# Performance work log

Measured on AMD Instinct MI355X. Metric: run time of the kernel, lower is better.

Reference implementation:

```python
import jax, jax.numpy as jnp
import numpy as np

B, T, F, H, E = 32, 512, 64, 64, 32  # batch, time, features(=sequence_length), hidden_dim, encoding_size


def setup_inputs() -> dict:
    key = jax.random.key(0)
    ks = jax.random.split(key, 14)
    sc = 0.05
    return {
        "x": jax.random.normal(ks[0], (B, T, F), jnp.float32),
        "s": jax.random.normal(ks[1], (B, T, E), jnp.float32),
        # gating FFN params
        "ffn_w1": jax.random.normal(ks[2], (F, H), jnp.float32) * sc,
        "ffn_b1": jnp.zeros((H,), jnp.float32),
        "ffn_w2": jax.random.normal(ks[3], (E, H), jnp.float32) * sc,
        "ffn_b2": jnp.zeros((H,), jnp.float32),
        "ffn_w3": jax.random.normal(ks[4], (H, F), jnp.float32) * sc,
        "ffn_b3": jnp.zeros((F,), jnp.float32),
        # per-feature expert FFN_j params (F experts, each Dense(1->H), ELU, Dense(H->H))
        "exp_w1": jax.random.normal(ks[5], (F, H), jnp.float32) * sc,  # weight of Dense(1->H) per feature
        "exp_b1": jnp.zeros((F, H), jnp.float32),
        "exp_w3": jax.random.normal(ks[6], (F, H, H), jnp.float32) * sc,
        "exp_b3": jnp.zeros((F, H), jnp.float32),
    }


def reference(x, s, ffn_w1, ffn_b1, ffn_w2, ffn_b2, ffn_w3, ffn_b3,
              exp_w1, exp_b1, exp_w3, exp_b3):
    # gating network: softmax over feature axis
    g = jnp.einsum('btf,fh->bth', x, ffn_w1) + ffn_b1 \
        + jnp.einsum('bte,eh->bth', s, ffn_w2) + ffn_b2
    logits = jnp.einsum('bth,hf->btf', jax.nn.elu(g), ffn_w3) + ffn_b3
    w_t = jax.nn.softmax(logits, axis=2)  # [B,T,F]

    # per-feature experts, batched: Dense(1->H) is a rank-1 outer product
    h = jax.nn.elu(x[..., None] * exp_w1[None, None] + exp_b1[None, None])  # [B,T,F,H]
    expert_out = jnp.einsum('btfh,fhk->btfk', h, exp_w3) + exp_b3[None, None]  # [B,T,F,H]

    # gate-weighted sum over features
    return jnp.einsum('btfk,btf->btk', expert_out, w_t)  # [B,T,H]
```

## Files before the change

kernel.cpp:

```cpp
#include <hip/hip_runtime.h>
#include <hip/hip_bf16.h>
#include <math.h>

#define NTOK 16384

typedef __attribute__((ext_vector_type(8))) short short8;
typedef __attribute__((ext_vector_type(4))) float f32x4;

__device__ __forceinline__ unsigned pack_bf16(float a, float b) {
    union { __hip_bfloat162 h; unsigned u; } cv;
    cv.h = __float22bfloat162_rn(make_float2(a, b));
    return cv.u;
}
__device__ __forceinline__ float eluf(float z) {
    return z > 0.0f ? z : (__expf(z) - 1.0f);
}

__global__ __launch_bounds__(256)
void prepass(const float* __restrict__ ew3, const float* __restrict__ eb3,
             unsigned short* __restrict__ ws) {
    __shared__ float tile[64 * 65];
    const int bid = blockIdx.x, tid = threadIdx.x;
    const float* src = (bid < 64) ? (ew3 + (size_t)bid * 4096) : eb3;

    const int r = tid >> 2, c0 = (tid & 3) * 16;
    #pragma unroll
    for (int j = 0; j < 4; ++j) {
        float4 v = *(const float4*)(src + r * 64 + c0 + j * 4);
        tile[r * 65 + c0 + j * 4 + 0] = v.x;
        tile[r * 65 + c0 + j * 4 + 1] = v.y;
        tile[r * 65 + c0 + j * 4 + 2] = v.z;
        tile[r * 65 + c0 + j * 4 + 3] = v.w;
    }
    __syncthreads();

    uint4* dst = (uint4*)(ws + (size_t)bid * 4096);
    #pragma unroll
    for (int it = 0; it < 2; ++it) {
        const int idx = tid + it * 256;
        const int c = idx >> 8, u = (idx >> 6) & 3, l = idx & 63;
        const int m = l & 15, q = (l >> 4) & 3;
        const int rb = c * 32 + q * 8, col = u * 16 + m;
        unsigned pw[4];
        #pragma unroll
        for (int p = 0; p < 4; ++p)
            pw[p] = pack_bf16(tile[(rb + 2 * p) * 65 + col],
                              tile[(rb + 2 * p + 1) * 65 + col]);
        uint4 pk; pk.x = pw[0]; pk.y = pw[1]; pk.z = pw[2]; pk.w = pw[3];
        dst[idx] = pk;
    }
}

__device__ __forceinline__ void gen_a(const float* __restrict__ ew1,
                                      const float* __restrict__ eb1,
                                      int f, int quad, float xv, float wt,
                                      short8* a) {
    #pragma unroll
    for (int c = 0; c < 2; ++c) {
        const float* w1p = ew1 + f * 64 + c * 32 + quad * 8;
        const float* b1p = eb1 + f * 64 + c * 32 + quad * 8;
        const float4 w1a = *(const float4*)w1p, w1b = *(const float4*)(w1p + 4);
        const float4 b1a = *(const float4*)b1p, b1b = *(const float4*)(b1p + 4);
        uint4 av;
        av.x = pack_bf16(wt * eluf(fmaf(xv, w1a.x, b1a.x)),
                         wt * eluf(fmaf(xv, w1a.y, b1a.y)));
        av.y = pack_bf16(wt * eluf(fmaf(xv, w1a.z, b1a.z)),
                         wt * eluf(fmaf(xv, w1a.w, b1a.w)));
        av.z = pack_bf16(wt * eluf(fmaf(xv, w1b.x, b1b.x)),
                         wt * eluf(fmaf(xv, w1b.y, b1b.y)));
        av.w = pack_bf16(wt * eluf(fmaf(xv, w1b.z, b1b.z)),
                         wt * eluf(fmaf(xv, w1b.w, b1b.w)));
        a[c] = *(short8*)&av;
    }
}

__device__ __forceinline__ void gen_b_fp32(const float* __restrict__ w3f,
                                           int quad, int m, short8 b[2][4]) {
    #pragma unroll
    for (int c = 0; c < 2; ++c)
        #pragma unroll
        for (int u = 0; u < 4; ++u) {
            const float* wp = w3f + (size_t)(c * 32 + quad * 8) * 64 + u * 16 + m;
            uint4 v;
            v.x = pack_bf16(wp[0],   wp[64]);
            v.y = pack_bf16(wp[128], wp[192]);
            v.z = pack_bf16(wp[256], wp[320]);
            v.w = pack_bf16(wp[384], wp[448]);
            b[c][u] = *(short8*)&v;
        }
}

__global__ __launch_bounds__(512, 8)
void moe_main(const float* __restrict__ x,   const float* __restrict__ s,
              const float* __restrict__ fw1, const float* __restrict__ fb1,
              const float* __restrict__ fw2, const float* __restrict__ fb2,
              const float* __restrict__ fw3, const float* __restrict__ fb3,
              const float* __restrict__ ew1, const float* __restrict__ eb1,
              const float* __restrict__ ew3, const float* __restrict__ eb3,
              const unsigned short* __restrict__ w3img, int use_ws,
              float* __restrict__ out)
{
    __shared__ __align__(16) float xls[16 * 68];
    __shared__ __align__(16) float wts[16 * 65];
    __shared__ __align__(16) float egs[16 * 64];
    __shared__ __align__(16) float ped[4][16 * 68];

    const int tid = threadIdx.x;
    const int wv = tid >> 6, lane = tid & 63;
    const int tokbase = blockIdx.x * 16;

    if (tid < 256) {
        const int t = tid >> 4, fq = (tid & 15) * 4;
        *(float4*)&xls[t * 68 + fq] =
            *(const float4*)(x + (size_t)(tokbase + t) * 64 + fq);
    }
    __syncthreads();

    {
        const int t0w = wv * 2;
        const float* sw = s + (size_t)(tokbase + t0w) * 32;
        float g0, g1;
        g0 = g1 = fb1[lane] + fb2[lane];
        for (int f = 0; f < 64; f += 4) {
            const float4 xa = *(const float4*)&xls[(t0w + 0) * 68 + f];
            const float4 xb = *(const float4*)&xls[(t0w + 1) * 68 + f];
            const float w0 = fw1[(f + 0) * 64 + lane];
            const float w1 = fw1[(f + 1) * 64 + lane];
            const float w2 = fw1[(f + 2) * 64 + lane];
            const float w3v = fw1[(f + 3) * 64 + lane];
            g0 = fmaf(xa.x, w0, fmaf(xa.y, w1, fmaf(xa.z, w2, fmaf(xa.w, w3v, g0))));
            g1 = fmaf(xb.x, w0, fmaf(xb.y, w1, fmaf(xb.z, w2, fmaf(xb.w, w3v, g1))));
        }
        for (int e = 0; e < 32; e += 4) {
            const float4 sa = *(const float4*)(sw + e);
            const float4 sb = *(const float4*)(sw + 32 + e);
            const float w0 = fw2[(e + 0) * 64 + lane];
            const float w1 = fw2[(e + 1) * 64 + lane];
            const float w2 = fw2[(e + 2) * 64 + lane];
            const float w3v = fw2[(e + 3) * 64 + lane];
            g0 = fmaf(sa.x, w0, fmaf(sa.y, w1, fmaf(sa.z, w2, fmaf(sa.w, w3v, g0))));
            g1 = fmaf(sb.x, w0, fmaf(sb.y, w1, fmaf(sb.z, w2, fmaf(sb.w, w3v, g1))));
        }
        egs[(t0w + 0) * 64 + lane] = eluf(g0);
        egs[(t0w + 1) * 64 + lane] = eluf(g1);
        __syncthreads();

        float lg0 = fb3[lane], lg1 = lg0;
        for (int h = 0; h < 64; h += 4) {
            const float4 e0 = *(const float4*)&egs[(t0w + 0) * 64 + h];
            const float4 e1 = *(const float4*)&egs[(t0w + 1) * 64 + h];
            const float w0 = fw3[(h + 0) * 64 + lane];
            const float w1 = fw3[(h + 1) * 64 + lane];
            const float w2 = fw3[(h + 2) * 64 + lane];
            const float w3v = fw3[(h + 3) * 64 + lane];
            lg0 = fmaf(e0.x, w0, fmaf(e0.y, w1, fmaf(e0.z, w2, fmaf(e0.w, w3v, lg0))));
            lg1 = fmaf(e1.x, w0, fmaf(e1.y, w1, fmaf(e1.z, w2, fmaf(e1.w, w3v, lg1))));
        }
        float mx0 = lg0, mx1 = lg1;
        #pragma unroll
        for (int off = 32; off > 0; off >>= 1) {
            mx0 = fmaxf(mx0, __shfl_xor(mx0, off));
            mx1 = fmaxf(mx1, __shfl_xor(mx1, off));
        }
        const float p0 = __expf(lg0 - mx0), p1 = __expf(lg1 - mx1);
        float s0 = p0, s1 = p1;
        #pragma unroll
        for (int off = 32; off > 0; off >>= 1) {
            s0 += __shfl_xor(s0, off);
            s1 += __shfl_xor(s1, off);
        }
        wts[(t0w + 0) * 65 + lane] = p0 / s0;
        wts[(t0w + 1) * 65 + lane] = p1 / s1;
    }
    __syncthreads();

    const int m = tid & 15, quad = (tid >> 4) & 3;
    const int f0 = wv * 8;

    f32x4 acc[4];
    #pragma unroll
    for (int u = 0; u < 4; ++u) acc[u] = (f32x4){0.f, 0.f, 0.f, 0.f};

    if (use_ws) {
        const uint4* bb = (const uint4*)w3img;
        #pragma unroll
        for (int ff = 0; ff < 8; ++ff) {
            const int f = f0 + ff;
            const uint4* bp = bb + (size_t)f * 512;
            const float xv = xls[m * 68 + f];
            const float wt = wts[m * 65 + f];
            short8 a[2];
            gen_a(ew1, eb1, f, quad, xv, wt, a);
            {
                uint4 b0 = bp[0 * 256 + 0 * 64 + lane];
                uint4 b1 = bp[0 * 256 + 1 * 64 + lane];
                uint4 b2 = bp[0 * 256 + 2 * 64 + lane];
                uint4 b3 = bp[0 * 256 + 3 * 64 + lane];
                acc[0] = __builtin_amdgcn_mfma_f32_16x16x32_bf16(a[0], *(short8*)&b0, acc[0], 0, 0, 0);
                acc[1] = __builtin_amdgcn_mfma_f32_16x16x32_bf16(a[0], *(short8*)&b1, acc[1], 0, 0, 0);
                acc[2] = __builtin_amdgcn_mfma_f32_16x16x32_bf16(a[0], *(short8*)&b2, acc[2], 0, 0, 0);
                acc[3] = __builtin_amdgcn_mfma_f32_16x16x32_bf16(a[0], *(short8*)&b3, acc[3], 0, 0, 0);
            }
            {
                uint4 b0 = bp[1 * 256 + 0 * 64 + lane];
                uint4 b1 = bp[1 * 256 + 1 * 64 + lane];
                uint4 b2 = bp[1 * 256 + 2 * 64 + lane];
                uint4 b3 = bp[1 * 256 + 3 * 64 + lane];
                acc[0] = __builtin_amdgcn_mfma_f32_16x16x32_bf16(a[1], *(short8*)&b0, acc[0], 0, 0, 0);
                acc[1] = __builtin_amdgcn_mfma_f32_16x16x32_bf16(a[1], *(short8*)&b1, acc[1], 0, 0, 0);
                acc[2] = __builtin_amdgcn_mfma_f32_16x16x32_bf16(a[1], *(short8*)&b2, acc[2], 0, 0, 0);
                acc[3] = __builtin_amdgcn_mfma_f32_16x16x32_bf16(a[1], *(short8*)&b3, acc[3], 0, 0, 0);
            }
        }
    } else {
        for (int ff = 0; ff < 8; ++ff) {
            const int f = f0 + ff;
            short8 b[2][4], a[2];
            gen_b_fp32(ew3 + (size_t)f * 4096, quad, m, b);
            gen_a(ew1, eb1, f, quad, xls[m * 68 + f], wts[m * 65 + f], a);
            #pragma unroll
            for (int u = 0; u < 4; ++u) {
                acc[u] = __builtin_amdgcn_mfma_f32_16x16x32_bf16(a[0], b[0][u], acc[u], 0, 0, 0);
                acc[u] = __builtin_amdgcn_mfma_f32_16x16x32_bf16(a[1], b[1][u], acc[u], 0, 0, 0);
            }
        }
    }

    if (wv < 2) {
        const int e0 = wv * 32 + quad * 8;
        uint4 av;
        av.x = pack_bf16(wts[m * 65 + e0 + 0], wts[m * 65 + e0 + 1]);
        av.y = pack_bf16(wts[m * 65 + e0 + 2], wts[m * 65 + e0 + 3]);
        av.z = pack_bf16(wts[m * 65 + e0 + 4], wts[m * 65 + e0 + 5]);
        av.w = pack_bf16(wts[m * 65 + e0 + 6], wts[m * 65 + e0 + 7]);
        short8 a = *(short8*)&av;
        short8 b[4];
        if (use_ws) {
            const uint4* bp = (const uint4*)(w3img + (size_t)64 * 4096);
            #pragma unroll
            for (int u = 0; u < 4; ++u) {
                uint4 bv = bp[wv * 256 + u * 64 + lane];
                b[u] = *(short8*)&bv;
            }
        } else {
            #pragma unroll
            for (int u = 0; u < 4; ++u) {
                const float* wp = eb3 + (size_t)e0 * 64 + u * 16 + m;
                uint4 bv;
                bv.x = pack_bf16(wp[0],   wp[64]);
                bv.y = pack_bf16(wp[128], wp[192]);
                bv.z = pack_bf16(wp[256], wp[320]);
                bv.w = pack_bf16(wp[384], wp[448]);
                b[u] = *(short8*)&bv;
            }
        }
        #pragma unroll
        for (int u = 0; u < 4; ++u)
            acc[u] = __builtin_amdgcn_mfma_f32_16x16x32_bf16(a, b[u], acc[u], 0, 0, 0);
    }

    if (wv >= 4) {
        #pragma unroll
        for (int u = 0; u < 4; ++u)
            #pragma unroll
            for (int r = 0; r < 4; ++r)
                ped[wv - 4][(quad * 4 + r) * 68 + u * 16 + m] = acc[u][r];
    }
    __syncthreads();
    if (wv < 4) {
        #pragma unroll
        for (int u = 0; u < 4; ++u)
            #pragma unroll
            for (int r = 0; r < 4; ++r)
                acc[u][r] += ped[wv][(quad * 4 + r) * 68 + u * 16 + m];
    }
    __syncthreads();
    if (wv == 2 || wv == 3) {
        #pragma unroll
        for (int u = 0; u < 4; ++u)
            #pragma unroll
            for (int r = 0; r < 4; ++r)
                ped[wv - 2][(quad * 4 + r) * 68 + u * 16 + m] = acc[u][r];
    }
    __syncthreads();
    if (wv < 2) {
        #pragma unroll
        for (int u = 0; u < 4; ++u)
            #pragma unroll
            for (int r = 0; r < 4; ++r)
                acc[u][r] += ped[wv][(quad * 4 + r) * 68 + u * 16 + m];
    }
    __syncthreads();
    if (wv == 1) {
        #pragma unroll
        for (int u = 0; u < 4; ++u)
            #pragma unroll
            for (int r = 0; r < 4; ++r)
                ped[0][(quad * 4 + r) * 68 + u * 16 + m] = acc[u][r];
    }
    __syncthreads();
    if (wv == 0) {
        #pragma unroll
        for (int u = 0; u < 4; ++u)
            #pragma unroll
            for (int r = 0; r < 4; ++r) {
                const int idx = (quad * 4 + r) * 68 + u * 16 + m;
                ped[0][idx] += acc[u][r];
            }
    }
    __syncthreads();

    if (tid < 256) {
        const int t = tid >> 4, kq = tid & 15;
        float4 o = *(const float4*)&ped[0][t * 68 + kq * 4];
        *(float4*)(out + (size_t)(tokbase + t) * 64 + kq * 4) = o;
    }
}

extern "C" void kernel_launch(void* const* d_in, const int* in_sizes, int n_in,
                              void* d_out, int out_size, void* d_ws, size_t ws_size,
                              hipStream_t stream) {
    const float* x   = (const float*)d_in[0];
    const float* s   = (const float*)d_in[1];
    const float* fw1 = (const float*)d_in[2];
    const float* fb1 = (const float*)d_in[3];
    const float* fw2 = (const float*)d_in[4];
    const float* fb2 = (const float*)d_in[5];
    const float* fw3 = (const float*)d_in[6];
    const float* fb3 = (const float*)d_in[7];
    const float* ew1 = (const float*)d_in[8];
    const float* eb1 = (const float*)d_in[9];
    const float* ew3 = (const float*)d_in[10];
    const float* eb3 = (const float*)d_in[11];
    float* out = (float*)d_out;

    const size_t ws_need = (size_t)65 * 4096 * sizeof(unsigned short);
    const int use_ws = (ws_size >= ws_need) && (((uintptr_t)d_ws & 15) == 0);
    unsigned short* w3img = (unsigned short*)d_ws;

    if (use_ws) prepass<<<dim3(65), dim3(256), 0, stream>>>(ew3, eb3, w3img);
    moe_main<<<dim3(NTOK / 16), dim3(512), 0, stream>>>(
        x, s, fw1, fb1, fw2, fb2, fw3, fb3, ew1, eb1, ew3, eb3,
        w3img, use_ws, out);
}
```

Baseline: 130.2 us.

## Split MoE into gate prep, feature-parallel expert kernel with register-resident weights, and reduction

Result: slower. 447.2 us (+243.5%).

```diff
diff --git a/kernel.cpp b/kernel.cpp
--- a/kernel.cpp
+++ b/kernel.cpp
@@ -3,6 +3,10 @@
 #include <math.h>
 
 #define NTOK 16384
+#define WTS_OFF   532480
+#define P_OFF     4726784
+#define NSLOT_F32 1048576
+#define WS_NEED   (size_t)(P_OFF + 9 * 4194304)
 
 typedef __attribute__((ext_vector_type(8))) short short8;
 typedef __attribute__((ext_vector_type(4))) float f32x4;
@@ -17,44 +21,275 @@
 }
 
 __global__ __launch_bounds__(256)
-void prepass(const float* __restrict__ ew3, const float* __restrict__ eb3,
-             unsigned short* __restrict__ ws) {
-    __shared__ float tile[64 * 65];
-    const int bid = blockIdx.x, tid = threadIdx.x;
-    const float* src = (bid < 64) ? (ew3 + (size_t)bid * 4096) : eb3;
-
-    const int r = tid >> 2, c0 = (tid & 3) * 16;
-    #pragma unroll
-    for (int j = 0; j < 4; ++j) {
-        float4 v = *(const float4*)(src + r * 64 + c0 + j * 4);
-        tile[r * 65 + c0 + j * 4 + 0] = v.x;
-        tile[r * 65 + c0 + j * 4 + 1] = v.y;
-        tile[r * 65 + c0 + j * 4 + 2] = v.z;
-        tile[r * 65 + c0 + j * 4 + 3] = v.w;
-    }
-    __syncthreads();
-
-    uint4* dst = (uint4*)(ws + (size_t)bid * 4096);
-    #pragma unroll
-    for (int it = 0; it < 2; ++it) {
-        const int idx = tid + it * 256;
-        const int c = idx >> 8, u = (idx >> 6) & 3, l = idx & 63;
-        const int m = l & 15, q = (l >> 4) & 3;
-        const int rb = c * 32 + q * 8, col = u * 16 + m;
-        unsigned pw[4];
-        #pragma unroll
-        for (int p = 0; p < 4; ++p)
-            pw[p] = pack_bf16(tile[(rb + 2 * p) * 65 + col],
-                              tile[(rb + 2 * p + 1) * 65 + col]);
-        uint4 pk; pk.x = pw[0]; pk.y = pw[1]; pk.z = pw[2]; pk.w = pw[3];
-        dst[idx] = pk;
-    }
-}
-
-__device__ __forceinline__ void gen_a(const float* __restrict__ ew1,
-                                      const float* __restrict__ eb1,
-                                      int f, int quad, float xv, float wt,
-                                      short8* a) {
+void gate_prep(const float* __restrict__ x,   const float* __restrict__ s,
+               const float* __restrict__ fw1, const float* __restrict__ fb1,
+               const float* __restrict__ fw2, const float* __restrict__ fb2,
+               const float* __restrict__ fw3, const float* __restrict__ fb3,
+               const float* __restrict__ ew3, const float* __restrict__ eb3,
+               unsigned short* __restrict__ img,
+               float* __restrict__ wtsb, float* __restrict__ p8)
+{
+    __shared__ __align__(16) float xls[16 * 68];
+    __shared__ __align__(16) float wts[16 * 65];
+    __shared__ __align__(16) float egs[16 * 64];
+    __shared__ __align__(16) float ptile[64 * 65];
+
+    const int tid = threadIdx.x, bid = blockIdx.x;
+
+    if (bid < 65) {
+        const float* src = (bid < 64) ? (ew3 + (size_t)bid * 4096) : eb3;
+        const int r = tid >> 2, c0 = (tid & 3) * 16;
+        #pragma unroll
+        for (int j = 0; j < 4; ++j) {
+            float4 v = *(const float4*)(src + r * 64 + c0 + j * 4);
+            ptile[r * 65 + c0 + j * 4 + 0] = v.x;
+            ptile[r * 65 + c0 + j * 4 + 1] = v.y;
+            ptile[r * 65 + c0 + j * 4 + 2] = v.z;
+            ptile[r * 65 + c0 + j * 4 + 3] = v.w;
+        }
+        __syncthreads();
+        uint4* dst = (uint4*)(img + (size_t)bid * 4096);
+        #pragma unroll
+        for (int it = 0; it < 2; ++it) {
+            const int idx = it * 256 + tid;
+            const int c = idx >> 8, u = (idx >> 6) & 3, l = idx & 63;
+            const int mm = l & 15, q = (l >> 4) & 3;
+            const int rb = c * 32 + q * 8, col = u * 16 + mm;
+            unsigned pw[4];
+            #pragma unroll
+            for (int p = 0; p < 4; ++p)
+                pw[p] = pack_bf16(ptile[(rb + 2 * p) * 65 + col],
+                                  ptile[(rb + 2 * p + 1) * 65 + col]);
+            uint4 pk; pk.x = pw[0]; pk.y = pw[1]; pk.z = pw[2]; pk.w = pw[3];
+            dst[idx] = pk;
+        }
+        return;
+    }
+
+    const int wv = tid >> 6, lane = tid & 63;
+    const int tokbase = (bid - 65) * 16;
+
+    if (tid < 256) {
+        const int t = tid >> 4, fq = (tid & 15) * 4;
+        *(float4*)&xls[t * 68 + fq] =
+            *(const float4*)(x + (size_t)(tokbase + t) * 64 + fq);
+    }
+    __syncthreads();
+
+    {
+        const int t0w = wv * 4;
+        const float* sw = s + (size_t)(tokbase + t0w) * 32;
+        float g[4];
+        const float b0 = fb1[lane] + fb2[lane];
+        #pragma unroll
+        for (int t = 0; t < 4; ++t) g[t] = b0;
+        for (int f = 0; f < 64; f += 4) {
+            const float w0 = fw1[(f + 0) * 64 + lane];
+            const float w1 = fw1[(f + 1) * 64 + lane];
+            const float w2 = fw1[(f + 2) * 64 + lane];
+            const float w3v = fw1[(f + 3) * 64 + lane];
+            #pragma unroll
+            for (int t = 0; t < 4; ++t) {
+                const float4 xa = *(const float4*)&xls[(t0w + t) * 68 + f];
+                g[t] = fmaf(xa.x, w0, fmaf(xa.y, w1, fmaf(xa.z, w2, fmaf(xa.w, w3v, g[t]))));
+            }
+        }
+        for (int e = 0; e < 32; e += 4) {
+            const float w0 = fw2[(e + 0) * 64 + lane];
+            const float w1 = fw2[(e + 1) * 64 + lane];
+            const float w2 = fw2[(e + 2) * 64 + lane];
+            const float w3v = fw2[(e + 3) * 64 + lane];
+            #pragma unroll
+            for (int t = 0; t < 4; ++t) {
+                const float4 sa = *(const float4*)(sw + t * 32 + e);
+                g[t] = fmaf(sa.x, w0, fmaf(sa.y, w1, fmaf(sa.z, w2, fmaf(sa.w, w3v, g[t]))));
+            }
+        }
+        #pragma unroll
+        for (int t = 0; t < 4; ++t) egs[(t0w + t) * 64 + lane] = eluf(g[t]);
+
+        float lg[4];
+        const float b3 = fb3[lane];
+        #pragma unroll
+        for (int t = 0; t < 4; ++t) lg[t] = b3;
+        for (int h = 0; h < 64; h += 4) {
+            const float w0 = fw3[(h + 0) * 64 + lane];
+            const float w1 = fw3[(h + 1) * 64 + lane];
+            const float w2 = fw3[(h + 2) * 64 + lane];
+            const float w3v = fw3[(h + 3) * 64 + lane];
+            #pragma unroll
+            for (int t = 0; t < 4; ++t) {
+                const float4 ev = *(const float4*)&egs[(t0w + t) * 64 + h];
+                lg[t] = fmaf(ev.x, w0, fmaf(ev.y, w1, fmaf(ev.z, w2, fmaf(ev.w, w3v, lg[t]))));
+            }
+        }
+        #pragma unroll
+        for (int t = 0; t < 4; ++t) {
+            float mx = lg[t];
+            #pragma unroll
+            for (int off = 32; off > 0; off >>= 1) mx = fmaxf(mx, __shfl_xor(mx, off));
+            const float p = __expf(lg[t] - mx);
+            float sm = p;
+            #pragma unroll
+            for (int off = 32; off > 0; off >>= 1) sm += __shfl_xor(sm, off);
+            const float w = p / sm;
+            wts[(t0w + t) * 65 + lane] = w;
+            wtsb[(size_t)(tokbase + t0w + t) * 64 + lane] = w;
+        }
+    }
+    __syncthreads();
+
+    const int m = tid & 15, quad = (tid >> 4) & 3;
+    f32x4 bacc[4];
+    #pragma unroll
+    for (int u = 0; u < 4; ++u) bacc[u] = (f32x4){0.f, 0.f, 0.f, 0.f};
+    if (wv < 2) {
+        const int e0 = wv * 32 + quad * 8;
+        uint4 av;
+        av.x = pack_bf16(wts[m * 65 + e0 + 0], wts[m * 65 + e0 + 1]);
+        av.y = pack_bf16(wts[m * 65 + e0 + 2], wts[m * 65 + e0 + 3]);
+        av.z = pack_bf16(wts[m * 65 + e0 + 4], wts[m * 65 + e0 + 5]);
+        av.w = pack_bf16(wts[m * 65 + e0 + 6], wts[m * 65 + e0 + 7]);
+        short8 a = *(short8*)&av;
+        #pragma unroll
+        for (int u = 0; u < 4; ++u) {
+            const float* wp = eb3 + (size_t)e0 * 64 + u * 16 + m;
+            uint4 bv;
+            bv.x = pack_bf16(wp[0],   wp[64]);
+            bv.y = pack_bf16(wp[128], wp[192]);
+            bv.z = pack_bf16(wp[256], wp[320]);
+            bv.w = pack_bf16(wp[384], wp[448]);
+            bacc[u] = __builtin_amdgcn_mfma_f32_16x16x32_bf16(a, *(short8*)&bv, bacc[u], 0, 0, 0);
+        }
+    }
+    if (wv == 1) {
+        #pragma unroll
+        for (int u = 0; u < 4; ++u)
+            #pragma unroll
+            for (int r = 0; r < 4; ++r)
+                xls[(quad * 4 + r) * 68 + u * 16 + m] = bacc[u][r];
+    }
+    __syncthreads();
+    if (wv == 0) {
+        #pragma unroll
+        for (int u = 0; u < 4; ++u)
+            #pragma unroll
+            for (int r = 0; r < 4; ++r) {
+                const int row = quad * 4 + r;
+                p8[(size_t)(tokbase + row) * 64 + u * 16 + m] =
+                    bacc[u][r] + xls[row * 68 + u * 16 + m];
+            }
+    }
+}
+
+__global__ __launch_bounds__(512, 4)
+void moe_pf(const float* __restrict__ x,
+            const float* __restrict__ ew1, const float* __restrict__ eb1,
+            const unsigned short* __restrict__ img,
+            const float* __restrict__ wtsb, float* __restrict__ part)
+{
+    __shared__ float accls[8 * 16 * 68];
+
+    const int tid = threadIdx.x, bid = blockIdx.x;
+    const int fg = bid & 7, tg = bid >> 3;
+    const int wv = tid >> 6, lane = tid & 63;
+    const int m = tid & 15, quad = (tid >> 4) & 3;
+    const int f = fg * 8 + wv;
+    const int t0 = tg * 128;
+
+    #pragma unroll
+    for (int k = 0; k < 17; ++k) accls[tid + k * 512] = 0.0f;
+    __syncthreads();
+
+    const uint4* bp = (const uint4*)img + (size_t)f * 512 + lane;
+    uint4 B[8];
+    #pragma unroll
+    for (int c = 0; c < 2; ++c)
+        #pragma unroll
+        for (int u = 0; u < 4; ++u) B[c * 4 + u] = bp[c * 256 + u * 64];
+
+    float w1r[16], b1r[16];
+    #pragma unroll
+    for (int c = 0; c < 2; ++c) {
+        const float4 wa = *(const float4*)(ew1 + f * 64 + c * 32 + quad * 8);
+        const float4 wb = *(const float4*)(ew1 + f * 64 + c * 32 + quad * 8 + 4);
+        const float4 ba = *(const float4*)(eb1 + f * 64 + c * 32 + quad * 8);
+        const float4 bb = *(const float4*)(eb1 + f * 64 + c * 32 + quad * 8 + 4);
+        w1r[c * 8 + 0] = wa.x; w1r[c * 8 + 1] = wa.y; w1r[c * 8 + 2] = wa.z; w1r[c * 8 + 3] = wa.w;
+        w1r[c * 8 + 4] = wb.x; w1r[c * 8 + 5] = wb.y; w1r[c * 8 + 6] = wb.z; w1r[c * 8 + 7] = wb.w;
+        b1r[c * 8 + 0] = ba.x; b1r[c * 8 + 1] = ba.y; b1r[c * 8 + 2] = ba.z; b1r[c * 8 + 3] = ba.w;
+        b1r[c * 8 + 4] = bb.x; b1r[c * 8 + 5] = bb.y; b1r[c * 8 + 6] = bb.z; b1r[c * 8 + 7] = bb.w;
+    }
+
+    float xc = x[(size_t)(t0 + m) * 64 + f];
+    float wc = wtsb[(size_t)(t0 + m) * 64 + f];
+    #pragma unroll
+    for (int tile = 0; tile < 8; ++tile) {
+        float xn = 0.f, wn = 0.f;
+        if (tile < 7) {
+            xn = x[(size_t)(t0 + (tile + 1) * 16 + m) * 64 + f];
+            wn = wtsb[(size_t)(t0 + (tile + 1) * 16 + m) * 64 + f];
+        }
+        short8 a[2];
+        #pragma unroll
+        for (int c = 0; c < 2; ++c) {
+            uint4 av;
+            av.x = pack_bf16(wc * eluf(fmaf(xc, w1r[c * 8 + 0], b1r[c * 8 + 0])),
+                             wc * eluf(fmaf(xc, w1r[c * 8 + 1], b1r[c * 8 + 1])));
+            av.y = pack_bf16(wc * eluf(fmaf(xc, w1r[c * 8 + 2], b1r[c * 8 + 2])),
+                             wc * eluf(fmaf(xc, w1r[c * 8 + 3], b1r[c * 8 + 3])));
+            av.z = pack_bf16(wc * eluf(fmaf(xc, w1r[c * 8 + 4], b1r[c * 8 + 4])),
+                             wc * eluf(fmaf(xc, w1r[c * 8 + 5], b1r[c * 8 + 5])));
+            av.w = pack_bf16(wc * eluf(fmaf(xc, w1r[c * 8 + 6], b1r[c * 8 + 6])),
+                             wc * eluf(fmaf(xc, w1r[c * 8 + 7], b1r[c * 8 + 7])));
+            a[c] = *(short8*)&av;
+        }
+        f32x4 acc[4];
+        #pragma unroll
+        for (int u = 0; u < 4; ++u) acc[u] = (f32x4){0.f, 0.f, 0.f, 0.f};
+        #pragma unroll
+        for (int u = 0; u < 4; ++u) {
+            acc[u] = __builtin_amdgcn_mfma_f32_16x16x32_bf16(a[0], *(short8*)&B[u],     acc[u], 0, 0, 0);
+            acc[u] = __builtin_amdgcn_mfma_f32_16x16x32_bf16(a[1], *(short8*)&B[4 + u], acc[u], 0, 0, 0);
+        }
+        float* ab = accls + tile * 1088;
+        #pragma unroll
+        for (int u = 0; u < 4; ++u)
+            #pragma unroll
+            for (int r = 0; r < 4; ++r)
+                atomicAdd(&ab[(quad * 4 + r) * 68 + u * 16 + m], acc[u][r]);
+        xc = xn; wc = wn;
+    }
+    __syncthreads();
+
+    float* pdst = part + (size_t)fg * NSLOT_F32 + (size_t)t0 * 64;
+    #pragma unroll
+    for (int k = 0; k < 4; ++k) {
+        const int j = tid + k * 512;
+        const int tile = j >> 8, rem = j & 255;
+        const int row = rem >> 4, cq = rem & 15;
+        float4 v = *(const float4*)&accls[tile * 1088 + row * 68 + cq * 4];
+        *(float4*)(pdst + (size_t)j * 4) = v;
+    }
+}
+
+__global__ __launch_bounds__(256)
+void reduce9(const float* __restrict__ part, float* __restrict__ out)
+{
+    const size_t i = ((size_t)blockIdx.x * 256 + threadIdx.x) * 4;
+    float4 s = *(const float4*)(part + i);
+    #pragma unroll
+    for (int sl = 1; sl < 9; ++sl) {
+        const float4 v = *(const float4*)(part + (size_t)sl * NSLOT_F32 + i);
+        s.x += v.x; s.y += v.y; s.z += v.z; s.w += v.w;
+    }
+    *(float4*)(out + i) = s;
+}
+
+__device__ __forceinline__ void gen_a_fb(const float* __restrict__ ew1,
+                                         const float* __restrict__ eb1,
+                                         int f, int quad, float xv, float wt,
+                                         short8* a) {
     #pragma unroll
     for (int c = 0; c < 2; ++c) {
         const float* w1p = ew1 + f * 64 + c * 32 + quad * 8;
@@ -73,7 +308,6 @@
         a[c] = *(short8*)&av;
     }
 }
-
 __device__ __forceinline__ void gen_b_fp32(const float* __restrict__ w3f,
                                            int quad, int m, short8 b[2][4]) {
     #pragma unroll
@@ -91,14 +325,13 @@
 }
 
 __global__ __launch_bounds__(512, 8)
-void moe_main(const float* __restrict__ x,   const float* __restrict__ s,
-              const float* __restrict__ fw1, const float* __restrict__ fb1,
-              const float* __restrict__ fw2, const float* __restrict__ fb2,
-              const float* __restrict__ fw3, const float* __restrict__ fb3,
-              const float* __restrict__ ew1, const float* __restrict__ eb1,
-              const float* __restrict__ ew3, const float* __restrict__ eb3,
-              const unsigned short* __restrict__ w3img, int use_ws,
-              float* __restrict__ out)
+void moe_fb(const float* __restrict__ x,   const float* __restrict__ s,
+            const float* __restrict__ fw1, const float* __restrict__ fb1,
+            const float* __restrict__ fw2, const float* __restrict__ fb2,
+            const float* __restrict__ fw3, const float* __restrict__ fb3,
+            const float* __restrict__ ew1, const float* __restrict__ eb1,
+            const float* __restrict__ ew3, const float* __restrict__ eb3,
+            float* __restrict__ out)
 {
     __shared__ __align__(16) float xls[16 * 68];
     __shared__ __align__(16) float wts[16 * 65];
@@ -115,19 +348,18 @@
             *(const float4*)(x + (size_t)(tokbase + t) * 64 + fq);
     }
     __syncthreads();
-
     {
         const int t0w = wv * 2;
         const float* sw = s + (size_t)(tokbase + t0w) * 32;
         float g0, g1;
         g0 = g1 = fb1[lane] + fb2[lane];
-        for (int f = 0; f < 64; f += 4) {
-            const float4 xa = *(const float4*)&xls[(t0w + 0) * 68 + f];
-            const float4 xb = *(const float4*)&xls[(t0w + 1) * 68 + f];
-            const float w0 = fw1[(f + 0) * 64 + lane];
-            const float w1 = fw1[(f + 1) * 64 + lane];
-            const float w2 = fw1[(f + 2) * 64 + lane];
-            const float w3v = fw1[(f + 3) * 64 + lane];
+        for (int ff = 0; ff < 64; ff += 4) {
+            const float4 xa = *(const float4*)&xls[(t0w + 0) * 68 + ff];
+            const float4 xb = *(const float4*)&xls[(t0w + 1) * 68 + ff];
+            const float w0 = fw1[(ff + 0) * 64 + lane];
+            const float w1 = fw1[(ff + 1) * 64 + lane];
+            const float w2 = fw1[(ff + 2) * 64 + lane];
+            const float w3v = fw1[(ff + 3) * 64 + lane];
             g0 = fmaf(xa.x, w0, fmaf(xa.y, w1, fmaf(xa.z, w2, fmaf(xa.w, w3v, g0))));
             g1 = fmaf(xb.x, w0, fmaf(xb.y, w1, fmaf(xb.z, w2, fmaf(xb.w, w3v, g1))));
         }
@@ -144,7 +376,6 @@
         egs[(t0w + 0) * 64 + lane] = eluf(g0);
         egs[(t0w + 1) * 64 + lane] = eluf(g1);
         __syncthreads();
-
         float lg0 = fb3[lane], lg1 = lg0;
         for (int h = 0; h < 64; h += 4) {
             const float4 e0 = *(const float4*)&egs[(t0w + 0) * 64 + h];
@@ -176,56 +407,21 @@
 
     const int m = tid & 15, quad = (tid >> 4) & 3;
     const int f0 = wv * 8;
-
     f32x4 acc[4];
     #pragma unroll
     for (int u = 0; u < 4; ++u) acc[u] = (f32x4){0.f, 0.f, 0.f, 0.f};
 
-    if (use_ws) {
-        const uint4* bb = (const uint4*)w3img;
-        #pragma unroll
-        for (int ff = 0; ff < 8; ++ff) {
-            const int f = f0 + ff;
-            const uint4* bp = bb + (size_t)f * 512;
-            const float xv = xls[m * 68 + f];
-            const float wt = wts[m * 65 + f];
-            short8 a[2];
-            gen_a(ew1, eb1, f, quad, xv, wt, a);
-            {
-                uint4 b0 = bp[0 * 256 + 0 * 64 + lane];
-                uint4 b1 = bp[0 * 256 + 1 * 64 + lane];
-                uint4 b2 = bp[0 * 256 + 2 * 64 + lane];
-                uint4 b3 = bp[0 * 256 + 3 * 64 + lane];
-                acc[0] = __builtin_amdgcn_mfma_f32_16x16x32_bf16(a[0], *(short8*)&b0, acc[0], 0, 0, 0);
-                acc[1] = __builtin_amdgcn_mfma_f32_16x16x32_bf16(a[0], *(short8*)&b1, acc[1], 0, 0, 0);
-                acc[2] = __builtin_amdgcn_mfma_f32_16x16x32_bf16(a[0], *(short8*)&b2, acc[2], 0, 0, 0);
-                acc[3] = __builtin_amdgcn_mfma_f32_16x16x32_bf16(a[0], *(short8*)&b3, acc[3], 0, 0, 0);
-            }
-            {
-                uint4 b0 = bp[1 * 256 + 0 * 64 + lane];
-                uint4 b1 = bp[1 * 256 + 1 * 64 + lane];
-                uint4 b2 = bp[1 * 256 + 2 * 64 + lane];
-                uint4 b3 = bp[1 * 256 + 3 * 64 + lane];
-                acc[0] = __builtin_amdgcn_mfma_f32_16x16x32_bf16(a[1], *(short8*)&b0, acc[0], 0, 0, 0);
-                acc[1] = __builtin_amdgcn_mfma_f32_16x16x32_bf16(a[1], *(short8*)&b1, acc[1], 0, 0, 0);
-                acc[2] = __builtin_amdgcn_mfma_f32_16x16x32_bf16(a[1], *(short8*)&b2, acc[2], 0, 0, 0);
-                acc[3] = __builtin_amdgcn_mfma_f32_16x16x32_bf16(a[1], *(short8*)&b3, acc[3], 0, 0, 0);
-            }
-        }
-    } else {
-        for (int ff = 0; ff < 8; ++ff) {
-            const int f = f0 + ff;
-            short8 b[2][4], a[2];
-            gen_b_fp32(ew3 + (size_t)f * 4096, quad, m, b);
-            gen_a(ew1, eb1, f, quad, xls[m * 68 + f], wts[m * 65 + f], a);
-            #pragma unroll
-            for (int u = 0; u < 4; ++u) {
-                acc[u] = __builtin_amdgcn_mfma_f32_16x16x32_bf16(a[0], b[0][u], acc[u], 0, 0, 0);
-                acc[u] = __builtin_amdgcn_mfma_f32_16x16x32_bf16(a[1], b[1][u], acc[u], 0, 0, 0);
-            }
-        }
-    }
-
+    for (int ff = 0; ff < 8; ++ff) {
+        const int fcur = f0 + ff;
+        short8 b[2][4], a[2];
+        gen_b_fp32(ew3 + (size_t)fcur * 4096, quad, m, b);
+        gen_a_fb(ew1, eb1, fcur, quad, xls[m * 68 + fcur], wts[m * 65 + fcur], a);
+        #pragma unroll
+        for (int u = 0; u < 4; ++u) {
+            acc[u] = __builtin_amdgcn_mfma_f32_16x16x32_bf16(a[0], b[0][u], acc[u], 0, 0, 0);
+            acc[u] = __builtin_amdgcn_mfma_f32_16x16x32_bf16(a[1], b[1][u], acc[u], 0, 0, 0);
+        }
+    }
     if (wv < 2) {
         const int e0 = wv * 32 + quad * 8;
         uint4 av;
@@ -234,31 +430,17 @@
         av.z = pack_bf16(wts[m * 65 + e0 + 4], wts[m * 65 + e0 + 5]);
         av.w = pack_bf16(wts[m * 65 + e0 + 6], wts[m * 65 + e0 + 7]);
         short8 a = *(short8*)&av;
-        short8 b[4];
-        if (use_ws) {
-            const uint4* bp = (const uint4*)(w3img + (size_t)64 * 4096);
-            #pragma unroll
-            for (int u = 0; u < 4; ++u) {
-                uint4 bv = bp[wv * 256 + u * 64 + lane];
-                b[u] = *(short8*)&bv;
-            }
-        } else {
-            #pragma unroll
-            for (int u = 0; u < 4; ++u) {
-                const float* wp = eb3 + (size_t)e0 * 64 + u * 16 + m;
-                uint4 bv;
-                bv.x = pack_bf16(wp[0],   wp[64]);
-                bv.y = pack_bf16(wp[128], wp[192]);
-                bv.z = pack_bf16(wp[256], wp[320]);
-                bv.w = pack_bf16(wp[384], wp[448]);
-                b[u] = *(short8*)&bv;
-            }
-        }
-        #pragma unroll
-        for (int u = 0; u < 4; ++u)
-            acc[u] = __builtin_amdgcn_mfma_f32_16x16x32_bf16(a, b[u], acc[u], 0, 0, 0);
-    }
-
+        #pragma unroll
+        for (int u = 0; u < 4; ++u) {
+            const float* wp = eb3 + (size_t)e0 * 64 + u * 16 + m;
+            uint4 bv;
+            bv.x = pack_bf16(wp[0],   wp[64]);
+            bv.y = pack_bf16(wp[128], wp[192]);
+            bv.z = pack_bf16(wp[256], wp[320]);
+            bv.w = pack_bf16(wp[384], wp[448]);
+            acc[u] = __builtin_amdgcn_mfma_f32_16x16x32_bf16(a, *(short8*)&bv, acc[u], 0, 0, 0);
+        }
+    }
     if (wv >= 4) {
         #pragma unroll
         for (int u = 0; u < 4; ++u)
@@ -303,13 +485,10 @@
         #pragma unroll
         for (int u = 0; u < 4; ++u)
             #pragma unroll
-            for (int r = 0; r < 4; ++r) {
-                const int idx = (quad * 4 + r) * 68 + u * 16 + m;
-                ped[0][idx] += acc[u][r];
-            }
-    }
-    __syncthreads();
-
+            for (int r = 0; r < 4; ++r)
+                ped[0][(quad * 4 + r) * 68 + u * 16 + m] += acc[u][r];
+    }
+    __syncthreads();
     if (tid < 256) {
         const int t = tid >> 4, kq = tid & 15;
         float4 o = *(const float4*)&ped[0][t * 68 + kq * 4];
@@ -334,12 +513,17 @@
     const float* eb3 = (const float*)d_in[11];
     float* out = (float*)d_out;
 
-    const size_t ws_need = (size_t)65 * 4096 * sizeof(unsigned short);
-    const int use_ws = (ws_size >= ws_need) && (((uintptr_t)d_ws & 15) == 0);
-    unsigned short* w3img = (unsigned short*)d_ws;
-
-    if (use_ws) prepass<<<dim3(65), dim3(256), 0, stream>>>(ew3, eb3, w3img);
-    moe_main<<<dim3(NTOK / 16), dim3(512), 0, stream>>>(
-        x, s, fw1, fb1, fw2, fb2, fw3, fb3, ew1, eb1, ew3, eb3,
-        w3img, use_ws, out);
-}
+    if (ws_size >= WS_NEED && (((uintptr_t)d_ws & 15) == 0)) {
+        unsigned short* img = (unsigned short*)d_ws;
+        float* wtsb = (float*)((char*)d_ws + WTS_OFF);
+        float* part = (float*)((char*)d_ws + P_OFF);
+        float* p8   = part + (size_t)8 * NSLOT_F32;
+        gate_prep<<<dim3(65 + NTOK / 16), dim3(256), 0, stream>>>(
+            x, s, fw1, fb1, fw2, fb2, fw3, fb3, ew3, eb3, img, wtsb, p8);
+        moe_pf<<<dim3(1024), dim3(512), 0, stream>>>(x, ew1, eb1, img, wtsb, part);
+        reduce9<<<dim3(1024), dim3(256), 0, stream>>>(part, out);
+    } else {
+        moe_fb<<<dim3(NTOK / 16), dim3(512), 0, stream>>>(
+            x, s, fw1, fb1, fw2, fb2, fw3, fb3, ew1, eb1, ew3, eb3, out);
+    }
+}
```
